# Kernel tuning notes

Measured on AMD Instinct MI355X. Metric: run time of the kernel, lower is better.

Reference implementation:

```python
import jax, jax.numpy as jnp
import numpy as np

B, L, D_MODEL, N_HEADS, M = 1, 2048, 512, 8, 128
D_HEAD = D_MODEL // N_HEADS
KERNEL_EPS = 1e-4
DENOM_EPS = 1e-6


def setup_inputs() -> dict:
    key = jax.random.key(0)
    ks = jax.random.split(key, 12)
    s = 0.02  # weight init scale
    return {
        "query": jax.random.normal(ks[0], (B, L, D_MODEL), jnp.float32),
        "key": jax.random.normal(ks[1], (B, L, D_MODEL), jnp.float32),
        "value": jax.random.normal(ks[2], (B, L, D_MODEL), jnp.float32),
        "Wq": jax.random.normal(ks[3], (D_MODEL, D_MODEL), jnp.float32) * s,
        "bq": jnp.zeros((D_MODEL,), jnp.float32),
        "Wk": jax.random.normal(ks[4], (D_MODEL, D_MODEL), jnp.float32) * s,
        "bk": jnp.zeros((D_MODEL,), jnp.float32),
        "Wv": jax.random.normal(ks[5], (D_MODEL, D_MODEL), jnp.float32) * s,
        "bv": jnp.zeros((D_MODEL,), jnp.float32),
        "Wo": jax.random.normal(ks[6], (D_MODEL, D_MODEL), jnp.float32) * s,
        "bo": jnp.zeros((D_MODEL,), jnp.float32),
        # FAVOR+ random feature matrix (d_head, m); treated as a fixed buffer
        "random_features": jax.random.normal(ks[7], (D_HEAD, M), jnp.float32),
    }


def reference(query, key, value, Wq, bq, Wk, bk, Wv, bv, Wo, bo, random_features):
    b, l, _ = query.shape

    def proj_split(x, W, bias):
        # nn.Linear: x @ W.T + b, then split heads -> (b, h, l, d_head)
        y = x @ W.T + bias
        return y.reshape(b, l, N_HEADS, D_HEAD).transpose(0, 2, 1, 3)

    q = proj_split(query, Wq, bq)
    k = proj_split(key, Wk, bk)
    v = proj_split(value, Wv, bv)

    # --- get_projected_queries_and_keys ('exp' kernel) ---
    scale = D_MODEL ** -0.25
    q = q * scale
    k = k * scale
    proj_q = q @ random_features  # (b, h, l, m)
    proj_k = k @ random_features
    h_q = -0.5 * jnp.sum(q * q, axis=-1, keepdims=True)  # (b, h, l, 1)
    h_k = -0.5 * jnp.sum(k * k, axis=-1, keepdims=True)
    # argmax over a size-1 last dim -> stabilizer is h_q itself (faithful to source)
    q_stab = h_q
    k_stab = jnp.max(h_k)  # global max, scalar
    nc = M ** -0.5
    q_prime = nc * (jnp.exp(h_q + (proj_q - q_stab)) + KERNEL_EPS)  # (b, h, l, m)
    k_prime = nc * (jnp.exp(h_k + (proj_k - k_stab)) + KERNEL_EPS)

    # --- causal numerator: per-head cumsum of k' (x) v outer products ---
    head_outs = []
    for h in range(N_HEADS):
        outer = jnp.einsum('blm,bld->blmd', k_prime[:, h], v[:, h])  # (b, l, m, d)
        prefix = jnp.cumsum(outer, axis=1)
        head_outs.append(jnp.einsum('blmd,blm->bld', prefix, q_prime[:, h]))
    numerator = jnp.stack(head_outs, axis=1)  # (b, h, l, d)

    # --- causal denominator: q' . cumsum(k') ---
    denom = jnp.einsum('bhlm,bhlm->bhl', q_prime, jnp.cumsum(k_prime, axis=2))
    context = numerator / (denom[..., None] + DENOM_EPS)

    # unshape and output projection
    context = context.transpose(0, 2, 1, 3).reshape(b, l, D_MODEL)
    return context @ Wo.T + bo
```

## Files before the change

### kernel.cpp

```cpp
#include <hip/hip_runtime.h>
#include <math.h>


#define L       2048
#define DMODEL  512
#define NH      8
#define DH      64
#define M       128
#define CT      64
#define NC      (L/CT)
#define KEPS    1e-4f
#define DEPS    1e-6f
#define SCALE   0.2102241038134286f
#define NCONST  0.08838834764831845f

#define OFF_VB     0
#define OFF_QPB    524288
#define OFF_KPB    1572864
#define OFF_SSB    2621440
#define OFF_SSZ    3670016
#define OFF_CTX    3702784
#define OFF_END    4227072

typedef short bf16x8 __attribute__((ext_vector_type(8)));
typedef float f32x4  __attribute__((ext_vector_type(4)));
typedef unsigned short ushort_t;

__device__ __forceinline__ ushort_t f2bf(float f) {
    unsigned u = __float_as_uint(f);
    return (ushort_t)((u + 0x7fffu + ((u >> 16) & 1u)) >> 16);
}
__device__ __forceinline__ float bf2f(ushort_t u) {
    return __uint_as_float(((unsigned)u) << 16);
}
__device__ __forceinline__ unsigned pack2(float a, float b) {
    return (unsigned)f2bf(a) | ((unsigned)f2bf(b) << 16);
}

__global__ __launch_bounds__(256) void qkvp_kernel(
    const float* __restrict__ xq, const float* __restrict__ xk, const float* __restrict__ xv,
    const float* __restrict__ Wq, const float* __restrict__ bq,
    const float* __restrict__ Wk, const float* __restrict__ bk,
    const float* __restrict__ Wv, const float* __restrict__ bv,
    const float* __restrict__ RF,
    ushort_t* __restrict__ Vb, ushort_t* __restrict__ QPb, ushort_t* __restrict__ KPb)
{
    __shared__ __align__(16) char smem[24832];
    __shared__ ushort_t Qt[64 * 136];
    __shared__ float ssq[128];
    uint4* As8 = (uint4*)smem;
    uint4* Bs8 = (uint4*)(smem + 520 * 16);
    ushort_t* RFTs = (ushort_t*)smem;

    const int tid  = threadIdx.x;
    const int lane = tid & 63;
    const int wave = tid >> 6;
    const int quad = lane >> 4;
    const int l15  = lane & 15;
    const int z = blockIdx.z;
    const int isK = (z == 1);
    const int row0 = blockIdx.x * 64;
    const int col0 = blockIdx.y * 128;

    const float* X; const float* W; const float* bias;
    if (z == 0)      { X = xq; W = Wq; bias = bq; }
    else if (z == 1) { X = xk; W = Wk; bias = bk; }
    else             { X = xv; W = Wv; bias = bv; }

    f32x4 acc[4][2];
    const f32x4 z4 = {0.f, 0.f, 0.f, 0.f};
    #pragma unroll
    for (int i = 0; i < 4; ++i) { acc[i][0] = z4; acc[i][1] = z4; }

    uint4 ra[2], rb[4];
    auto loadA = [&](int ck) {
        #pragma unroll
        for (int it = 0; it < 2; ++it) {
            int t = tid + it * 256;
            int row = t >> 3, k8 = t & 7;
            const float4* gp = (const float4*)&X[(row0 + row) * DMODEL + ck * 64 + k8 * 8];
            float4 v0 = gp[0], v1 = gp[1];
            ra[it] = make_uint4(pack2(v0.x, v0.y), pack2(v0.z, v0.w),
                                pack2(v1.x, v1.y), pack2(v1.z, v1.w));
        }
    };
    auto loadB = [&](int ck) {
        #pragma unroll
        for (int it = 0; it < 4; ++it) {
            int t = tid + it * 256;
            int col = t >> 3, k8 = t & 7;
            const float4* gp = (const float4*)&W[(col0 + col) * DMODEL + ck * 64 + k8 * 8];
            float4 v0 = gp[0], v1 = gp[1];
            rb[it] = make_uint4(pack2(v0.x, v0.y), pack2(v0.z, v0.w),
                                pack2(v1.x, v1.y), pack2(v1.z, v1.w));
        }
    };

    loadA(0); loadB(0);
    const int wn = wave;
    for (int ck = 0; ck < 8; ++ck) {
        __syncthreads();
        #pragma unroll
        for (int it = 0; it < 2; ++it) {
            int t = tid + it * 256;
            As8[(t & 7) * 65 + (t >> 3)] = ra[it];
        }
        #pragma unroll
        for (int it = 0; it < 4; ++it) {
            int t = tid + it * 256;
            Bs8[(t & 7) * 129 + (t >> 3)] = rb[it];
        }
        __syncthreads();
        if (ck < 7) { loadA(ck + 1); loadB(ck + 1); }
        const bf16x8* Av = (const bf16x8*)As8;
        const bf16x8* Bv = (const bf16x8*)Bs8;
        #pragma unroll
        for (int kc = 0; kc < 2; ++kc) {
            const int k8 = kc * 4 + quad;
            bf16x8 af[4], bfr[2];
            #pragma unroll
            for (int i = 0; i < 4; ++i) af[i] = Av[k8 * 65 + i * 16 + l15];
            #pragma unroll
            for (int j = 0; j < 2; ++j) bfr[j] = Bv[k8 * 129 + wn * 32 + j * 16 + l15];
            #pragma unroll
            for (int i = 0; i < 4; ++i)
                #pragma unroll
                for (int j = 0; j < 2; ++j)
                    acc[i][j] = __builtin_amdgcn_mfma_f32_16x16x32_bf16(af[i], bfr[j], acc[i][j], 0, 0, 0);
        }
    }

    if (z == 2) {
        #pragma unroll
        for (int i = 0; i < 4; ++i)
            #pragma unroll
            for (int j = 0; j < 2; ++j) {
                int c = col0 + wn * 32 + j * 16 + l15;
                float bv_ = bias[c];
                #pragma unroll
                for (int reg = 0; reg < 4; ++reg) {
                    int r = row0 + i * 16 + quad * 4 + reg;
                    Vb[r * DMODEL + c] = f2bf(acc[i][j][reg] + bv_);
                }
            }
        return;
    }

    #pragma unroll
    for (int i = 0; i < 4; ++i)
        #pragma unroll
        for (int j = 0; j < 2; ++j) {
            int c = wn * 32 + j * 16 + l15;
            float bv_ = bias[col0 + c];
            #pragma unroll
            for (int reg = 0; reg < 4; ++reg) {
                int r = i * 16 + quad * 4 + reg;
                Qt[r * 136 + c] = f2bf(acc[i][j][reg] + bv_);
            }
        }
    __syncthreads();

    {
        int m = tid & 127, half = tid >> 7;
        #pragma unroll
        for (int j = 0; j < 32; ++j) {
            int d = half * 32 + j;
            RFTs[m * 72 + d] = f2bf(SCALE * RF[d * M + m]);
        }
    }
    if (isK && tid < 128) {
        int hh = tid >> 6, row = tid & 63;
        float s = 0.f;
        #pragma unroll
        for (int d = 0; d < DH; ++d) {
            float v = bf2f(Qt[row * 136 + hh * 64 + d]);
            s += v * v;
        }
        ssq[tid] = s;
    }
    __syncthreads();

    const int hh = wave >> 1, mh = wave & 1;
    const float s2h = 0.5f * SCALE * SCALE;
    f32x4 pac[4][4];
    #pragma unroll
    for (int i = 0; i < 4; ++i)
        #pragma unroll
        for (int j = 0; j < 4; ++j) pac[i][j] = z4;
    #pragma unroll
    for (int kc = 0; kc < 2; ++kc) {
        bf16x8 af[4], bfr[4];
        #pragma unroll
        for (int i = 0; i < 4; ++i)
            af[i] = *(const bf16x8*)&Qt[(i * 16 + l15) * 136 + hh * 64 + kc * 32 + quad * 8];
        #pragma unroll
        for (int j = 0; j < 4; ++j)
            bfr[j] = *(const bf16x8*)&RFTs[(mh * 64 + j * 16 + l15) * 72 + kc * 32 + quad * 8];
        #pragma unroll
        for (int i = 0; i < 4; ++i)
            #pragma unroll
            for (int j = 0; j < 4; ++j)
                pac[i][j] = __builtin_amdgcn_mfma_f32_16x16x32_bf16(af[i], bfr[j], pac[i][j], 0, 0, 0);
    }

    ushort_t* dst = isK ? KPb : QPb;
    const int hgl = blockIdx.y * 2 + hh;
    #pragma unroll
    for (int i = 0; i < 4; ++i)
        #pragma unroll
        for (int reg = 0; reg < 4; ++reg) {
            int row = i * 16 + quad * 4 + reg;
            float off = isK ? (-s2h * ssq[hh * 64 + row]) : 0.f;
            #pragma unroll
            for (int j = 0; j < 4; ++j) {
                int m = mh * 64 + j * 16 + l15;
                float p = pac[i][j][reg] + off;
                dst[((long)hgl * L + row0 + row) * M + m] = f2bf(NCONST * (expf(p) + KEPS));
            }
        }
}

__global__ __launch_bounds__(256) void out_gemm_kernel(
    const ushort_t* __restrict__ ctxb, const float* __restrict__ Wo,
    const float* __restrict__ bo, float* __restrict__ out)
{
    __shared__ uint4 As8[8 * 33];
    __shared__ uint4 Bs8[8 * 129];
    const int tid  = threadIdx.x;
    const int lane = tid & 63;
    const int wn   = tid >> 6;
    const int quad = lane >> 4;
    const int l15  = lane & 15;
    const int row0 = blockIdx.x * 32;
    const int col0 = blockIdx.y * 128;

    f32x4 acc[2][2];
    const f32x4 z4 = {0.f, 0.f, 0.f, 0.f};
    acc[0][0] = z4; acc[0][1] = z4; acc[1][0] = z4; acc[1][1] = z4;

    uint4 ra, rb[4];
    auto loadA = [&](int ck) {
        int row = tid >> 3, k8 = tid & 7;
        ra = *(const uint4*)&ctxb[(row0 + row) * DMODEL + ck * 64 + k8 * 8];
    };
    auto loadB = [&](int ck) {
        #pragma unroll
        for (int it = 0; it < 4; ++it) {
            int t = tid + it * 256;
            int col = t >> 3, k8 = t & 7;
            const float4* gp = (const float4*)&Wo[(col0 + col) * DMODEL + ck * 64 + k8 * 8];
            float4 v0 = gp[0], v1 = gp[1];
            rb[it] = make_uint4(pack2(v0.x, v0.y), pack2(v0.z, v0.w),
                                pack2(v1.x, v1.y), pack2(v1.z, v1.w));
        }
    };

    loadA(0); loadB(0);
    for (int ck = 0; ck < 8; ++ck) {
        __syncthreads();
        As8[(tid & 7) * 33 + (tid >> 3)] = ra;
        #pragma unroll
        for (int it = 0; it < 4; ++it) {
            int t = tid + it * 256;
            Bs8[(t & 7) * 129 + (t >> 3)] = rb[it];
        }
        __syncthreads();
        if (ck < 7) { loadA(ck + 1); loadB(ck + 1); }
        const bf16x8* Av = (const bf16x8*)As8;
        const bf16x8* Bv = (const bf16x8*)Bs8;
        #pragma unroll
        for (int kc = 0; kc < 2; ++kc) {
            const int k8 = kc * 4 + quad;
            bf16x8 af[2], bfr[2];
            af[0] = Av[k8 * 33 + l15];
            af[1] = Av[k8 * 33 + 16 + l15];
            #pragma unroll
            for (int j = 0; j < 2; ++j) bfr[j] = Bv[k8 * 129 + wn * 32 + j * 16 + l15];
            #pragma unroll
            for (int i = 0; i < 2; ++i)
                #pragma unroll
                for (int j = 0; j < 2; ++j)
                    acc[i][j] = __builtin_amdgcn_mfma_f32_16x16x32_bf16(af[i], bfr[j], acc[i][j], 0, 0, 0);
        }
    }
    #pragma unroll
    for (int i = 0; i < 2; ++i)
        #pragma unroll
        for (int j = 0; j < 2; ++j) {
            int c = col0 + wn * 32 + j * 16 + l15;
            float bv_ = bo[c];
            #pragma unroll
            for (int reg = 0; reg < 4; ++reg) {
                int r = row0 + i * 16 + quad * 4 + reg;
                out[r * DMODEL + c] = acc[i][j][reg] + bv_;
            }
        }
}

__global__ __launch_bounds__(256) void chunksum_mfma_kernel(
    const ushort_t* __restrict__ KPb, const ushort_t* __restrict__ Vb,
    ushort_t* __restrict__ SSb, float* __restrict__ SSz)
{
    __shared__ ushort_t Kt[128 * 72];
    __shared__ ushort_t Vt[80 * 72];
    const int tid = threadIdx.x;
    const int c = blockIdx.x, h = blockIdx.y;
    const int lane = tid & 63;
    const int wave = tid >> 6;
    const int quad = lane >> 4, l15 = lane & 15;
    const int t = lane, g = wave;

    {
        const ushort_t* kr = &KPb[((long)(h * L) + c * CT + t) * M];
        #pragma unroll
        for (int it = 0; it < 4; ++it) {
            int mo = it * 4 + g;
            uint4 u = *(const uint4*)&kr[mo * 8];
            ushort_t e[8] = {(ushort_t)(u.x & 0xffff), (ushort_t)(u.x >> 16),
                             (ushort_t)(u.y & 0xffff), (ushort_t)(u.y >> 16),
                             (ushort_t)(u.z & 0xffff), (ushort_t)(u.z >> 16),
                             (ushort_t)(u.w & 0xffff), (ushort_t)(u.w >> 16)};
            #pragma unroll
            for (int j = 0; j < 8; ++j) Kt[(mo * 8 + j) * 72 + t] = e[j];
        }
        const ushort_t* vr = &Vb[(c * CT + t) * DMODEL + h * DH];
        #pragma unroll
        for (int it = 0; it < 2; ++it) {
            int dd = it * 4 + g;
            uint4 u = *(const uint4*)&vr[dd * 8];
            ushort_t e[8] = {(ushort_t)(u.x & 0xffff), (ushort_t)(u.x >> 16),
                             (ushort_t)(u.y & 0xffff), (ushort_t)(u.y >> 16),
                             (ushort_t)(u.z & 0xffff), (ushort_t)(u.z >> 16),
                             (ushort_t)(u.w & 0xffff), (ushort_t)(u.w >> 16)};
            #pragma unroll
            for (int j = 0; j < 8; ++j) Vt[(dd * 8 + j) * 72 + t] = e[j];
        }
        if (g == 0) Vt[64 * 72 + t] = 0x3F80;
        if (g == 1) {
            #pragma unroll
            for (int r = 65; r < 80; ++r) Vt[r * 72 + t] = 0;
        }
    }
    __syncthreads();

    f32x4 acc[2][5];
    const f32x4 z4 = {0.f, 0.f, 0.f, 0.f};
    #pragma unroll
    for (int i = 0; i < 2; ++i)
        #pragma unroll
        for (int j = 0; j < 5; ++j) acc[i][j] = z4;
    #pragma unroll
    for (int kt = 0; kt < 2; ++kt) {
        bf16x8 af[2], bfr[5];
        #pragma unroll
        for (int i = 0; i < 2; ++i)
            af[i] = *(const bf16x8*)&Kt[(wave * 32 + i * 16 + l15) * 72 + kt * 32 + quad * 8];
        #pragma unroll
        for (int j = 0; j < 5; ++j)
            bfr[j] = *(const bf16x8*)&Vt[(j * 16 + l15) * 72 + kt * 32 + quad * 8];
        #pragma unroll
        for (int i = 0; i < 2; ++i)
            #pragma unroll
            for (int j = 0; j < 5; ++j)
                acc[i][j] = __builtin_amdgcn_mfma_f32_16x16x32_bf16(af[i], bfr[j], acc[i][j], 0, 0, 0);
    }
    ushort_t* outS = SSb + (long)(h * NC + c) * 8192;
    #pragma unroll
    for (int i = 0; i < 2; ++i)
        #pragma unroll
        for (int reg = 0; reg < 4; ++reg) {
            int m = wave * 32 + i * 16 + quad * 4 + reg;
            #pragma unroll
            for (int j = 0; j < 4; ++j)
                outS[m * 64 + j * 16 + l15] = f2bf(acc[i][j][reg]);
            if (l15 == 0) SSz[(h * NC + c) * M + m] = acc[i][4][reg];
        }
}

__global__ __launch_bounds__(256) void prefix_kernel(
    ushort_t* __restrict__ SSb, float* __restrict__ SSz)
{
    const int h = blockIdx.y;
    if (blockIdx.x == 32) {
        const int m = threadIdx.x;
        if (m < M) {
            float v[NC];
            #pragma unroll
            for (int c = 0; c < NC; ++c) v[c] = SSz[(h * NC + c) * M + m];
            float run = 0.f;
            #pragma unroll
            for (int c = 0; c < NC; ++c) {
                SSz[(h * NC + c) * M + m] = run;
                run += v[c];
            }
        }
        return;
    }
    const int idx = blockIdx.x * 256 + threadIdx.x;
    ushort_t v[NC];
    #pragma unroll
    for (int c = 0; c < NC; ++c) v[c] = SSb[(long)(h * NC + c) * 8192 + idx];
    float run = 0.f;
    #pragma unroll
    for (int c = 0; c < NC; ++c) {
        SSb[(long)(h * NC + c) * 8192 + idx] = f2bf(run);
        run += bf2f(v[c]);
    }
}

__global__ __launch_bounds__(512) void attn_kernel(
    const ushort_t* __restrict__ QPb, const ushort_t* __restrict__ KPb,
    const ushort_t* __restrict__ Vb, const ushort_t* __restrict__ SSb,
    const float* __restrict__ SSz, ushort_t* __restrict__ ctxb)
{
    __shared__ ushort_t Qp[64 * 136];
    __shared__ ushort_t Kp[64 * 136];
    __shared__ ushort_t St[80 * 136];
    __shared__ ushort_t Vt[80 * 72];
    __shared__ ushort_t Am[64 * 72];
    __shared__ float den[CT];
    const int tid = threadIdx.x;
    const int c = blockIdx.x, h = blockIdx.y;
    const int lane = tid & 63;
    const int wave = tid >> 6;
    const int i  = wave & 3;
    const int nh = wave >> 2;
    const int quad = lane >> 4;
    const int l15  = lane & 15;

    for (int t = tid; t < 2048; t += 512) {
        int mat = t >> 10, r = (t >> 4) & 63, c8 = t & 15;
        const ushort_t* src = mat ? KPb : QPb;
        uint4 u = *(const uint4*)&src[((long)(h * L) + c * CT + r) * M + c8 * 8];
        ushort_t* dst = mat ? Kp : Qp;
        *(uint4*)&dst[r * 136 + c8 * 8] = u;
    }
    {
        int t = tid & 63, dg = tid >> 6;
        uint4 u = *(const uint4*)&Vb[(c * CT + t) * DMODEL + h * DH + dg * 8];
        ushort_t e[8] = {(ushort_t)(u.x & 0xffff), (ushort_t)(u.x >> 16),
                         (ushort_t)(u.y & 0xffff), (ushort_t)(u.y >> 16),
                         (ushort_t)(u.z & 0xffff), (ushort_t)(u.z >> 16),
                         (ushort_t)(u.w & 0xffff), (ushort_t)(u.w >> 16)};
        #pragma unroll
        for (int j = 0; j < 8; ++j) Vt[(dg * 8 + j) * 72 + t] = e[j];
    }
    {
        const ushort_t* ssb = SSb + (long)(h * NC + c) * 8192;
        int m = tid & 127, dg = tid >> 7;
        #pragma unroll
        for (int it = 0; it < 2; ++it) {
            int dd = it * 4 + dg;
            uint4 u = *(const uint4*)&ssb[m * 64 + dd * 8];
            ushort_t e[8] = {(ushort_t)(u.x & 0xffff), (ushort_t)(u.x >> 16),
                             (ushort_t)(u.y & 0xffff), (ushort_t)(u.y >> 16),
                             (ushort_t)(u.z & 0xffff), (ushort_t)(u.z >> 16),
                             (ushort_t)(u.w & 0xffff), (ushort_t)(u.w >> 16)};
            #pragma unroll
            for (int j = 0; j < 8; ++j) St[(dd * 8 + j) * 136 + m] = e[j];
        }
    }
    if (tid < 128) St[64 * 136 + tid] = f2bf(SSz[(h * NC + c) * M + tid]);
    if (tid >= 128 && tid < 192) Vt[64 * 72 + (tid - 128)] = 0x3F80;
    for (int t = tid; t < 15 * 136; t += 512) St[65 * 136 + t] = 0;
    for (int t = tid; t < 15 * 72; t += 512)  Vt[65 * 72 + t] = 0;
    __syncthreads();

    f32x4 acc1[2];
    const f32x4 z4 = {0.f, 0.f, 0.f, 0.f};
    acc1[0] = z4; acc1[1] = z4;
    #pragma unroll
    for (int kt = 0; kt < 4; ++kt) {
        bf16x8 af = *(const bf16x8*)&Qp[(i * 16 + l15) * 136 + kt * 32 + quad * 8];
        #pragma unroll
        for (int jt = 0; jt < 2; ++jt) {
            bf16x8 bf = *(const bf16x8*)&Kp[(nh * 32 + jt * 16 + l15) * 136 + kt * 32 + quad * 8];
            acc1[jt] = __builtin_amdgcn_mfma_f32_16x16x32_bf16(af, bf, acc1[jt], 0, 0, 0);
        }
    }
    #pragma unroll
    for (int jt = 0; jt < 2; ++jt) {
        int col = nh * 32 + jt * 16 + l15;
        #pragma unroll
        for (int reg = 0; reg < 4; ++reg) {
            int row = i * 16 + quad * 4 + reg;
            Am[row * 72 + col] = f2bf((col <= row) ? acc1[jt][reg] : 0.f);
        }
    }
    __syncthreads();

    f32x4 acc2[2], acc3;
    acc2[0] = z4; acc2[1] = z4; acc3 = z4;
    #pragma unroll
    for (int kt = 0; kt < 6; ++kt) {
        bf16x8 af = (kt < 2)
            ? *(const bf16x8*)&Am[(i * 16 + l15) * 72 + kt * 32 + quad * 8]
            : *(const bf16x8*)&Qp[(i * 16 + l15) * 136 + (kt - 2) * 32 + quad * 8];
        #pragma unroll
        for (int jt = 0; jt < 2; ++jt) {
            int n = nh * 32 + jt * 16 + l15;
            bf16x8 bf = (kt < 2)
                ? *(const bf16x8*)&Vt[n * 72 + kt * 32 + quad * 8]
                : *(const bf16x8*)&St[n * 136 + (kt - 2) * 32 + quad * 8];
            acc2[jt] = __builtin_amdgcn_mfma_f32_16x16x32_bf16(af, bf, acc2[jt], 0, 0, 0);
        }
        if (nh == 0) {
            bf16x8 bz = (kt < 2)
                ? *(const bf16x8*)&Vt[(64 + l15) * 72 + kt * 32 + quad * 8]
                : *(const bf16x8*)&St[(64 + l15) * 136 + (kt - 2) * 32 + quad * 8];
            acc3 = __builtin_amdgcn_mfma_f32_16x16x32_bf16(af, bz, acc3, 0, 0, 0);
        }
    }
    if (nh == 0 && l15 == 0) {
        #pragma unroll
        for (int reg = 0; reg < 4; ++reg)
            den[i * 16 + quad * 4 + reg] = acc3[reg];
    }
    __syncthreads();
    #pragma unroll
    for (int jt = 0; jt < 2; ++jt) {
        int d = nh * 32 + jt * 16 + l15;
        #pragma unroll
        for (int reg = 0; reg < 4; ++reg) {
            int row = i * 16 + quad * 4 + reg;
            ctxb[(c * CT + row) * DMODEL + h * DH + d] = f2bf(acc2[jt][reg] / (den[row] + DEPS));
        }
    }
}

extern "C" void kernel_launch(void* const* d_in, const int* in_sizes, int n_in,
                              void* d_out, int out_size, void* d_ws, size_t ws_size,
                              hipStream_t stream)
{
    const float* query = (const float*)d_in[0];
    const float* key_  = (const float*)d_in[1];
    const float* value = (const float*)d_in[2];
    const float* Wq = (const float*)d_in[3];
    const float* bq = (const float*)d_in[4];
    const float* Wk = (const float*)d_in[5];
    const float* bk = (const float*)d_in[6];
    const float* Wv = (const float*)d_in[7];
    const float* bv = (const float*)d_in[8];
    const float* Wo = (const float*)d_in[9];
    const float* bo = (const float*)d_in[10];
    const float* RF = (const float*)d_in[11];

    float* ws = (float*)d_ws;
    ushort_t* Vb   = (ushort_t*)(ws + OFF_VB);
    ushort_t* QPb  = (ushort_t*)(ws + OFF_QPB);
    ushort_t* KPb  = (ushort_t*)(ws + OFF_KPB);
    ushort_t* SSb  = (ushort_t*)(ws + OFF_SSB);
    float* SSz     = ws + OFF_SSZ;
    ushort_t* CTXB = (ushort_t*)(ws + OFF_CTX);

    qkvp_kernel<<<dim3(32, 4, 3), 256, 0, stream>>>(query, key_, value,
                                                    Wq, bq, Wk, bk, Wv, bv, RF,
                                                    Vb, QPb, KPb);
    chunksum_mfma_kernel<<<dim3(NC, 8), 256, 0, stream>>>(KPb, Vb, SSb, SSz);
    prefix_kernel<<<dim3(33, 8), 256, 0, stream>>>(SSb, SSz);
    attn_kernel<<<dim3(NC, 8), 512, 0, stream>>>(QPb, KPb, Vb, SSb, SSz, CTXB);
    out_gemm_kernel<<<dim3(64, 4), 256, 0, stream>>>(CTXB, Wo, bo, (float*)d_out);
}
```

Before: 138.2 us.

## Fuse V projection and chunk-sum computation into the K projection blocks

```diff
diff --git a/kernel.cpp b/kernel.cpp
--- a/kernel.cpp
+++ b/kernel.cpp
@@ -43,14 +43,17 @@
     const float* __restrict__ Wk, const float* __restrict__ bk,
     const float* __restrict__ Wv, const float* __restrict__ bv,
     const float* __restrict__ RF,
-    ushort_t* __restrict__ Vb, ushort_t* __restrict__ QPb, ushort_t* __restrict__ KPb)
+    ushort_t* __restrict__ Vb, ushort_t* __restrict__ QPb, ushort_t* __restrict__ KPb,
+    ushort_t* __restrict__ SSb, float* __restrict__ SSz)
 {
     __shared__ __align__(16) char smem[24832];
     __shared__ ushort_t Qt[64 * 136];
+    __shared__ ushort_t Kt[128 * 72];
     __shared__ float ssq[128];
     uint4* As8 = (uint4*)smem;
     uint4* Bs8 = (uint4*)(smem + 520 * 16);
     ushort_t* RFTs = (ushort_t*)smem;
+    ushort_t* Vt2  = (ushort_t*)smem;
 
     const int tid  = threadIdx.x;
     const int lane = tid & 63;
@@ -61,90 +64,75 @@
     const int isK = (z == 1);
     const int row0 = blockIdx.x * 64;
     const int col0 = blockIdx.y * 128;
+    const int wn = wave;
+    const f32x4 z4 = {0.f, 0.f, 0.f, 0.f};
 
     const float* X; const float* W; const float* bias;
-    if (z == 0)      { X = xq; W = Wq; bias = bq; }
-    else if (z == 1) { X = xk; W = Wk; bias = bk; }
-    else             { X = xv; W = Wv; bias = bv; }
-
-    f32x4 acc[4][2];
-    const f32x4 z4 = {0.f, 0.f, 0.f, 0.f};
-    #pragma unroll
-    for (int i = 0; i < 4; ++i) { acc[i][0] = z4; acc[i][1] = z4; }
+    if (z == 0) { X = xq; W = Wq; bias = bq; }
+    else        { X = xk; W = Wk; bias = bk; }
 
     uint4 ra[2], rb[4];
-    auto loadA = [&](int ck) {
+    auto loadA = [&](const float* P, int ck) {
         #pragma unroll
         for (int it = 0; it < 2; ++it) {
             int t = tid + it * 256;
             int row = t >> 3, k8 = t & 7;
-            const float4* gp = (const float4*)&X[(row0 + row) * DMODEL + ck * 64 + k8 * 8];
+            const float4* gp = (const float4*)&P[(row0 + row) * DMODEL + ck * 64 + k8 * 8];
             float4 v0 = gp[0], v1 = gp[1];
             ra[it] = make_uint4(pack2(v0.x, v0.y), pack2(v0.z, v0.w),
                                 pack2(v1.x, v1.y), pack2(v1.z, v1.w));
         }
     };
-    auto loadB = [&](int ck) {
+    auto loadB = [&](const float* P, int ck) {
         #pragma unroll
         for (int it = 0; it < 4; ++it) {
             int t = tid + it * 256;
             int col = t >> 3, k8 = t & 7;
-            const float4* gp = (const float4*)&W[(col0 + col) * DMODEL + ck * 64 + k8 * 8];
+            const float4* gp = (const float4*)&P[(col0 + col) * DMODEL + ck * 64 + k8 * 8];
             float4 v0 = gp[0], v1 = gp[1];
             rb[it] = make_uint4(pack2(v0.x, v0.y), pack2(v0.z, v0.w),
                                 pack2(v1.x, v1.y), pack2(v1.z, v1.w));
         }
     };
-
-    loadA(0); loadB(0);
-    const int wn = wave;
-    for (int ck = 0; ck < 8; ++ck) {
-        __syncthreads();
-        #pragma unroll
-        for (int it = 0; it < 2; ++it) {
-            int t = tid + it * 256;
-            As8[(t & 7) * 65 + (t >> 3)] = ra[it];
-        }
-        #pragma unroll
-        for (int it = 0; it < 4; ++it) {
-            int t = tid + it * 256;
-            Bs8[(t & 7) * 129 + (t >> 3)] = rb[it];
-        }
-        __syncthreads();
-        if (ck < 7) { loadA(ck + 1); loadB(ck + 1); }
-        const bf16x8* Av = (const bf16x8*)As8;
-        const bf16x8* Bv = (const bf16x8*)Bs8;
-        #pragma unroll
-        for (int kc = 0; kc < 2; ++kc) {
-            const int k8 = kc * 4 + quad;
-            bf16x8 af[4], bfr[2];
-            #pragma unroll
-            for (int i = 0; i < 4; ++i) af[i] = Av[k8 * 65 + i * 16 + l15];
-            #pragma unroll
-            for (int j = 0; j < 2; ++j) bfr[j] = Bv[k8 * 129 + wn * 32 + j * 16 + l15];
-            #pragma unroll
-            for (int i = 0; i < 4; ++i)
-                #pragma unroll
-                for (int j = 0; j < 2; ++j)
-                    acc[i][j] = __builtin_amdgcn_mfma_f32_16x16x32_bf16(af[i], bfr[j], acc[i][j], 0, 0, 0);
-        }
-    }
-
-    if (z == 2) {
-        #pragma unroll
-        for (int i = 0; i < 4; ++i)
-            #pragma unroll
-            for (int j = 0; j < 2; ++j) {
-                int c = col0 + wn * 32 + j * 16 + l15;
-                float bv_ = bias[c];
-                #pragma unroll
-                for (int reg = 0; reg < 4; ++reg) {
-                    int r = row0 + i * 16 + quad * 4 + reg;
-                    Vb[r * DMODEL + c] = f2bf(acc[i][j][reg] + bv_);
-                }
-            }
-        return;
-    }
+    auto run_gemm = [&](const float* Xp, const float* Wp, f32x4 (&acc)[4][2]) {
+        #pragma unroll
+        for (int i = 0; i < 4; ++i) { acc[i][0] = z4; acc[i][1] = z4; }
+        loadA(Xp, 0); loadB(Wp, 0);
+        for (int ck = 0; ck < 8; ++ck) {
+            __syncthreads();
+            #pragma unroll
+            for (int it = 0; it < 2; ++it) {
+                int t = tid + it * 256;
+                As8[(t & 7) * 65 + (t >> 3)] = ra[it];
+            }
+            #pragma unroll
+            for (int it = 0; it < 4; ++it) {
+                int t = tid + it * 256;
+                Bs8[(t & 7) * 129 + (t >> 3)] = rb[it];
+            }
+            __syncthreads();
+            if (ck < 7) { loadA(Xp, ck + 1); loadB(Wp, ck + 1); }
+            const bf16x8* Av = (const bf16x8*)As8;
+            const bf16x8* Bv = (const bf16x8*)Bs8;
+            #pragma unroll
+            for (int kc = 0; kc < 2; ++kc) {
+                const int k8 = kc * 4 + quad;
+                bf16x8 af[4], bfr[2];
+                #pragma unroll
+                for (int i = 0; i < 4; ++i) af[i] = Av[k8 * 65 + i * 16 + l15];
+                #pragma unroll
+                for (int j = 0; j < 2; ++j) bfr[j] = Bv[k8 * 129 + wn * 32 + j * 16 + l15];
+                #pragma unroll
+                for (int i = 0; i < 4; ++i)
+                    #pragma unroll
+                    for (int j = 0; j < 2; ++j)
+                        acc[i][j] = __builtin_amdgcn_mfma_f32_16x16x32_bf16(af[i], bfr[j], acc[i][j], 0, 0, 0);
+            }
+        }
+    };
+
+    f32x4 acc[4][2];
+    run_gemm(X, W, acc);
 
     #pragma unroll
     for (int i = 0; i < 4; ++i)
@@ -158,6 +146,23 @@
                 Qt[r * 136 + c] = f2bf(acc[i][j][reg] + bv_);
             }
         }
+
+    f32x4 acc2[4][2];
+    if (isK) {
+        run_gemm(xv, Wv, acc2);
+        #pragma unroll
+        for (int i = 0; i < 4; ++i)
+            #pragma unroll
+            for (int j = 0; j < 2; ++j) {
+                int c = col0 + wn * 32 + j * 16 + l15;
+                float bv_ = bv[c];
+                #pragma unroll
+                for (int reg = 0; reg < 4; ++reg) {
+                    int r = row0 + i * 16 + quad * 4 + reg;
+                    Vb[r * DMODEL + c] = f2bf(acc2[i][j][reg] + bv_);
+                }
+            }
+    }
     __syncthreads();
 
     {
@@ -203,21 +208,100 @@
                 pac[i][j] = __builtin_amdgcn_mfma_f32_16x16x32_bf16(af[i], bfr[j], pac[i][j], 0, 0, 0);
     }
 
-    ushort_t* dst = isK ? KPb : QPb;
-    const int hgl = blockIdx.y * 2 + hh;
+    if (!isK) {
+        const int hgl = blockIdx.y * 2 + hh;
+        #pragma unroll
+        for (int i = 0; i < 4; ++i)
+            #pragma unroll
+            for (int reg = 0; reg < 4; ++reg) {
+                int row = i * 16 + quad * 4 + reg;
+                #pragma unroll
+                for (int j = 0; j < 4; ++j) {
+                    int m = mh * 64 + j * 16 + l15;
+                    float p = pac[i][j][reg];
+                    QPb[((long)hgl * L + row0 + row) * M + m] = f2bf(NCONST * (expf(p) + KEPS));
+                }
+            }
+        return;
+    }
+
+    __syncthreads();
     #pragma unroll
     for (int i = 0; i < 4; ++i)
         #pragma unroll
-        for (int reg = 0; reg < 4; ++reg) {
-            int row = i * 16 + quad * 4 + reg;
-            float off = isK ? (-s2h * ssq[hh * 64 + row]) : 0.f;
-            #pragma unroll
-            for (int j = 0; j < 4; ++j) {
-                int m = mh * 64 + j * 16 + l15;
-                float p = pac[i][j][reg] + off;
-                dst[((long)hgl * L + row0 + row) * M + m] = f2bf(NCONST * (expf(p) + KEPS));
-            }
-        }
+        for (int j = 0; j < 2; ++j) {
+            int c = wn * 32 + j * 16 + l15;
+            int head = c >> 6, d = c & 63;
+            float bv_ = bv[col0 + c];
+            #pragma unroll
+            for (int reg = 0; reg < 4; ++reg) {
+                int t = i * 16 + quad * 4 + reg;
+                Vt2[head * 5760 + d * 72 + t] = f2bf(acc2[i][j][reg] + bv_);
+            }
+        }
+    {
+        if (wave < 2) Vt2[wave * 5760 + 64 * 72 + lane] = 0x3F80;
+        for (int t = tid; t < 2 * 15 * 72; t += 256) {
+            int head = t / (15 * 72), r = t % (15 * 72);
+            Vt2[head * 5760 + 65 * 72 + r] = 0;
+        }
+    }
+
+    const int cchunk = blockIdx.x;
+    for (int hh2 = 0; hh2 < 2; ++hh2) {
+        __syncthreads();
+        if (hh == hh2) {
+            const int hgl = blockIdx.y * 2 + hh;
+            #pragma unroll
+            for (int i = 0; i < 4; ++i)
+                #pragma unroll
+                for (int reg = 0; reg < 4; ++reg) {
+                    int t = i * 16 + quad * 4 + reg;
+                    float off = -s2h * ssq[hh * 64 + t];
+                    #pragma unroll
+                    for (int j = 0; j < 4; ++j) {
+                        int m = mh * 64 + j * 16 + l15;
+                        ushort_t kp = f2bf(NCONST * (expf(pac[i][j][reg] + off) + KEPS));
+                        KPb[((long)hgl * L + row0 + t) * M + m] = kp;
+                        Kt[m * 72 + t] = kp;
+                    }
+                }
+        }
+        __syncthreads();
+        f32x4 cs[2][5];
+        #pragma unroll
+        for (int i = 0; i < 2; ++i)
+            #pragma unroll
+            for (int j = 0; j < 5; ++j) cs[i][j] = z4;
+        const ushort_t* vtp = &Vt2[hh2 * 5760];
+        #pragma unroll
+        for (int kt = 0; kt < 2; ++kt) {
+            bf16x8 af[2], bfr[5];
+            #pragma unroll
+            for (int i = 0; i < 2; ++i)
+                af[i] = *(const bf16x8*)&Kt[(wave * 32 + i * 16 + l15) * 72 + kt * 32 + quad * 8];
+            #pragma unroll
+            for (int j = 0; j < 5; ++j)
+                bfr[j] = *(const bf16x8*)&vtp[(j * 16 + l15) * 72 + kt * 32 + quad * 8];
+            #pragma unroll
+            for (int i = 0; i < 2; ++i)
+                #pragma unroll
+                for (int j = 0; j < 5; ++j)
+                    cs[i][j] = __builtin_amdgcn_mfma_f32_16x16x32_bf16(af[i], bfr[j], cs[i][j], 0, 0, 0);
+        }
+        const int hgl2 = blockIdx.y * 2 + hh2;
+        ushort_t* outS = SSb + (long)(hgl2 * NC + cchunk) * 8192;
+        #pragma unroll
+        for (int i = 0; i < 2; ++i)
+            #pragma unroll
+            for (int reg = 0; reg < 4; ++reg) {
+                int m = wave * 32 + i * 16 + quad * 4 + reg;
+                #pragma unroll
+                for (int j = 0; j < 4; ++j)
+                    outS[m * 64 + j * 16 + l15] = f2bf(cs[i][j][reg]);
+                if (l15 == 0) SSz[(hgl2 * NC + cchunk) * M + m] = cs[i][4][reg];
+            }
+    }
 }
 
 __global__ __launch_bounds__(256) void out_gemm_kernel(
@@ -294,86 +378,6 @@
                 int r = row0 + i * 16 + quad * 4 + reg;
                 out[r * DMODEL + c] = acc[i][j][reg] + bv_;
             }
-        }
-}
-
-__global__ __launch_bounds__(256) void chunksum_mfma_kernel(
-    const ushort_t* __restrict__ KPb, const ushort_t* __restrict__ Vb,
-    ushort_t* __restrict__ SSb, float* __restrict__ SSz)
-{
-    __shared__ ushort_t Kt[128 * 72];
-    __shared__ ushort_t Vt[80 * 72];
-    const int tid = threadIdx.x;
-    const int c = blockIdx.x, h = blockIdx.y;
-    const int lane = tid & 63;
-    const int wave = tid >> 6;
-    const int quad = lane >> 4, l15 = lane & 15;
-    const int t = lane, g = wave;
-
-    {
-        const ushort_t* kr = &KPb[((long)(h * L) + c * CT + t) * M];
-        #pragma unroll
-        for (int it = 0; it < 4; ++it) {
-            int mo = it * 4 + g;
-            uint4 u = *(const uint4*)&kr[mo * 8];
-            ushort_t e[8] = {(ushort_t)(u.x & 0xffff), (ushort_t)(u.x >> 16),
-                             (ushort_t)(u.y & 0xffff), (ushort_t)(u.y >> 16),
-                             (ushort_t)(u.z & 0xffff), (ushort_t)(u.z >> 16),
-                             (ushort_t)(u.w & 0xffff), (ushort_t)(u.w >> 16)};
-            #pragma unroll
-            for (int j = 0; j < 8; ++j) Kt[(mo * 8 + j) * 72 + t] = e[j];
-        }
-        const ushort_t* vr = &Vb[(c * CT + t) * DMODEL + h * DH];
-        #pragma unroll
-        for (int it = 0; it < 2; ++it) {
-            int dd = it * 4 + g;
-            uint4 u = *(const uint4*)&vr[dd * 8];
-            ushort_t e[8] = {(ushort_t)(u.x & 0xffff), (ushort_t)(u.x >> 16),
-                             (ushort_t)(u.y & 0xffff), (ushort_t)(u.y >> 16),
-                             (ushort_t)(u.z & 0xffff), (ushort_t)(u.z >> 16),
-                             (ushort_t)(u.w & 0xffff), (ushort_t)(u.w >> 16)};
-            #pragma unroll
-            for (int j = 0; j < 8; ++j) Vt[(dd * 8 + j) * 72 + t] = e[j];
-        }
-        if (g == 0) Vt[64 * 72 + t] = 0x3F80;
-        if (g == 1) {
-            #pragma unroll
-            for (int r = 65; r < 80; ++r) Vt[r * 72 + t] = 0;
-        }
-    }
-    __syncthreads();
-
-    f32x4 acc[2][5];
-    const f32x4 z4 = {0.f, 0.f, 0.f, 0.f};
-    #pragma unroll
-    for (int i = 0; i < 2; ++i)
-        #pragma unroll
-        for (int j = 0; j < 5; ++j) acc[i][j] = z4;
-    #pragma unroll
-    for (int kt = 0; kt < 2; ++kt) {
-        bf16x8 af[2], bfr[5];
-        #pragma unroll
-        for (int i = 0; i < 2; ++i)
-            af[i] = *(const bf16x8*)&Kt[(wave * 32 + i * 16 + l15) * 72 + kt * 32 + quad * 8];
-        #pragma unroll
-        for (int j = 0; j < 5; ++j)
-            bfr[j] = *(const bf16x8*)&Vt[(j * 16 + l15) * 72 + kt * 32 + quad * 8];
-        #pragma unroll
-        for (int i = 0; i < 2; ++i)
-            #pragma unroll
-            for (int j = 0; j < 5; ++j)
-                acc[i][j] = __builtin_amdgcn_mfma_f32_16x16x32_bf16(af[i], bfr[j], acc[i][j], 0, 0, 0);
-    }
-    ushort_t* outS = SSb + (long)(h * NC + c) * 8192;
-    #pragma unroll
-    for (int i = 0; i < 2; ++i)
-        #pragma unroll
-        for (int reg = 0; reg < 4; ++reg) {
-            int m = wave * 32 + i * 16 + quad * 4 + reg;
-            #pragma unroll
-            for (int j = 0; j < 4; ++j)
-                outS[m * 64 + j * 16 + l15] = f2bf(acc[i][j][reg]);
-            if (l15 == 0) SSz[(h * NC + c) * M + m] = acc[i][4][reg];
         }
 }
 
@@ -553,10 +557,9 @@
     float* SSz     = ws + OFF_SSZ;
     ushort_t* CTXB = (ushort_t*)(ws + OFF_CTX);
 
-    qkvp_kernel<<<dim3(32, 4, 3), 256, 0, stream>>>(query, key_, value,
+    qkvp_kernel<<<dim3(32, 4, 2), 256, 0, stream>>>(query, key_, value,
                                                     Wq, bq, Wk, bk, Wv, bv, RF,
-                                                    Vb, QPb, KPb);
-    chunksum_mfma_kernel<<<dim3(NC, 8), 256, 0, stream>>>(KPb, Vb, SSb, SSz);
+                                                    Vb, QPb, KPb, SSb, SSz);
     prefix_kernel<<<dim3(33, 8), 256, 0, stream>>>(SSb, SSz);
     attn_kernel<<<dim3(NC, 8), 512, 0, stream>>>(QPb, KPb, Vb, SSb, SSz, CTXB);
     out_gemm_kernel<<<dim3(64, 4), 256, 0, stream>>>(CTXB, Wo, bo, (float*)d_out);
```

Result: no change. 139.1 us (+0.7%).
